# Kernel tuning notes

Measured on AMD Instinct MI355X. Metric: run time of the kernel, lower is better.

## Reference

```python
import jax, jax.numpy as jnp
import numpy as np

D_MODEL = 768
N_HEADS = 12
D_HEAD = D_MODEL // N_HEADS

def setup_inputs() -> dict:
    key = jax.random.key(0)
    ks = jax.random.split(key, 5)
    B, T = 2, 4096
    x = jax.random.normal(ks[0], (B, T, D_MODEL), dtype=jnp.float32)
    s_in = 1.0 / np.sqrt(D_MODEL)
    W_qkv = jax.random.normal(ks[1], (D_MODEL, 3 * D_MODEL), dtype=jnp.float32) * s_in
    b_qkv = jnp.zeros((3 * D_MODEL,), dtype=jnp.float32)
    W_proj = jax.random.normal(ks[2], (D_MODEL, D_MODEL), dtype=jnp.float32) * s_in
    b_proj = jnp.zeros((D_MODEL,), dtype=jnp.float32)
    return {"x": x, "W_qkv": W_qkv, "b_qkv": b_qkv, "W_proj": W_proj, "b_proj": b_proj}

def reference(x, W_qkv, b_qkv, W_proj, b_proj):
    B, T, C = x.shape
    qkv = x @ W_qkv + b_qkv                      # [B,T,3C]
    q, k, v = jnp.split(qkv, 3, axis=-1)
    def heads(t):
        return t.reshape(B, T, N_HEADS, D_HEAD).transpose(0, 2, 1, 3)  # [B,H,T,d]
    q, k, v = heads(q), heads(k), heads(v)
    scale = 1.0 / np.sqrt(D_HEAD)
    att = jnp.einsum('bhqd,bhkd->bhqk', q, k) * scale  # [B,H,T,T]
    causal = jnp.tril(jnp.ones((T, T), dtype=bool))
    att = jnp.where(causal[None, None], att, -jnp.inf)
    att = jax.nn.softmax(att, axis=-1)
    y = jnp.einsum('bhqk,bhkd->bhqd', att, v)          # [B,H,T,d]
    y = y.transpose(0, 2, 1, 3).reshape(B, T, C)
    return y @ W_proj + b_proj
```

## Files before the change

kernel.cpp:

```cpp
#include <hip/hip_runtime.h>
#include <hip/hip_bf16.h>

typedef __bf16 bf16_t;
typedef bf16_t bf16x4 __attribute__((ext_vector_type(4)));
typedef bf16_t bf16x8 __attribute__((ext_vector_type(8)));
typedef float  f32x4  __attribute__((ext_vector_type(4)));

#define TSEQ   4096
#define NBATCH 2
#define DMODEL 768
#define NHEADS 12
#define DHEAD  64
#define NTOK   (NBATCH*TSEQ)
#define NQKV   (3*DMODEL)

#define QSCALE 0.18033688011112042f
#define SMAX 24.0f

__device__ __forceinline__ f32x4 mfma16(bf16x8 a, bf16x8 b, f32x4 c) {
  return __builtin_amdgcn_mfma_f32_16x16x32_bf16(a, b, c, 0, 0, 0);
}

__device__ __forceinline__ void glds16(const bf16_t* g, bf16_t* l) {
  __builtin_amdgcn_global_load_lds(
      (const __attribute__((address_space(1))) void*)g,
      (__attribute__((address_space(3))) void*)l, 16, 0, 0);
}
__device__ __forceinline__ void glds16f(const float* g, float* l) {
  __builtin_amdgcn_global_load_lds(
      (const __attribute__((address_space(1))) void*)g,
      (__attribute__((address_space(3))) void*)l, 16, 0, 0);
}

__global__ __launch_bounds__(256) void k_transpose_cvt2(
    const float* __restrict__ W1, bf16_t* __restrict__ O1,
    const float* __restrict__ W2, bf16_t* __restrict__ O2) {
  __shared__ bf16_t tile[64][66];
  int t = blockIdx.x;
  const float* in; bf16_t* out; int R, C, c0, r0;
  if (t < 432) { in = W1; out = O1; R = DMODEL; C = NQKV;
                 c0 = (t % 36) * 64; r0 = (t / 36) * 64; }
  else { t -= 432; in = W2; out = O2; R = DMODEL; C = DMODEL;
         c0 = (t % 12) * 64; r0 = (t / 12) * 64; }
  const int tid = threadIdx.x;
  const int r = tid >> 2, cb = (tid & 3) * 16;
  const float* ip = in + (long)(r0 + r) * C + c0 + cb;
#pragma unroll
  for (int k = 0; k < 16; k += 4) {
    float4 v = *(const float4*)(ip + k);
    tile[r][cb + k + 0] = (bf16_t)v.x;
    tile[r][cb + k + 1] = (bf16_t)v.y;
    tile[r][cb + k + 2] = (bf16_t)v.z;
    tile[r][cb + k + 3] = (bf16_t)v.w;
  }
  __syncthreads();
  const int c = tid >> 2, rb = (tid & 3) * 16;
  bf16_t* op = out + (long)(c0 + c) * R + r0 + rb;
  bf16x8 v0, v1;
#pragma unroll
  for (int i = 0; i < 8; ++i) { v0[i] = tile[rb + i][c]; v1[i] = tile[rb + 8 + i][c]; }
  *(bf16x8*)(op) = v0;
  *(bf16x8*)(op + 8) = v1;
}

__global__ __launch_bounds__(256) void k_gemm_qkv(
    const float* __restrict__ X, const bf16_t* __restrict__ Bt,
    const float* __restrict__ bias,
    bf16_t* __restrict__ Qo, bf16_t* __restrict__ Ko, bf16_t* __restrict__ Vt) {
  __shared__ __align__(16) float  Asf[2 * 128 * 32];
  __shared__ __align__(16) bf16_t Bs[2 * 128 * 32];
  const int wave = threadIdx.x >> 6;
  const int lane = threadIdx.x & 63;
  const int quad = lane >> 4;
  const int l16  = lane & 15;
  const int m0 = blockIdx.x * 128;
  const int n0 = blockIdx.y * 128;

  const int arow = lane >> 3;
  const int achk = (lane & 7) ^ arow;
  const float* x0 = X + (long)(m0 + wave * 8 + arow) * DMODEL + achk * 4;
  const int srow = lane >> 2;
  const int scol = (lane & 3) * 8;
  const bf16_t* b0 = Bt + (long)(n0 + wave * 16 + srow) * DMODEL + scol;

  f32x4 acc[2][8] = {};

#pragma unroll
  for (int i = 0; i < 4; ++i)
    glds16f(x0 + (long)i * 32 * DMODEL, Asf + (i * 32 + wave * 8) * 32);
  glds16(b0,               Bs + wave * 16 * 32);
  glds16(b0 + 64 * DMODEL, Bs + (64 + wave * 16) * 32);
  __syncthreads();

  const int sk = l16 & 7;
  for (int ks = 0; ks < DMODEL / 32; ++ks) {
    const int p = ks & 1;
    if (ks + 1 < DMODEL / 32) {
      const int k1 = (ks + 1) * 32;
      float*  Asx = (p ? Asf : Asf + 128 * 32);
      bf16_t* Bsx = (p ? Bs : Bs + 128 * 32);
#pragma unroll
      for (int i = 0; i < 4; ++i)
        glds16f(x0 + (long)i * 32 * DMODEL + k1, Asx + (i * 32 + wave * 8) * 32);
      glds16(b0 + k1,               Bsx + wave * 16 * 32);
      glds16(b0 + 64 * DMODEL + k1, Bsx + (64 + wave * 16) * 32);
    }
    const float*  Ap = Asf + p * (128 * 32);
    const bf16_t* Bp = Bs + p * (128 * 32);

    const int r0 = wave * 32 + l16, r1 = r0 + 16;
    f32x4 a0lo = *(const f32x4*)(Ap + r0 * 32 + (((2 * quad)     ^ sk) << 2));
    f32x4 a0hi = *(const f32x4*)(Ap + r0 * 32 + (((2 * quad + 1) ^ sk) << 2));
    f32x4 a1lo = *(const f32x4*)(Ap + r1 * 32 + (((2 * quad)     ^ sk) << 2));
    f32x4 a1hi = *(const f32x4*)(Ap + r1 * 32 + (((2 * quad + 1) ^ sk) << 2));
    bf16x8 af0, af1;
#pragma unroll
    for (int j = 0; j < 4; ++j) {
      af0[j] = (bf16_t)a0lo[j]; af0[4 + j] = (bf16_t)a0hi[j];
      af1[j] = (bf16_t)a1lo[j]; af1[4 + j] = (bf16_t)a1hi[j];
    }
#pragma unroll
    for (int nt = 0; nt < 8; ++nt) {
      bf16x8 bfm = *(const bf16x8*)(Bp + (nt * 16 + l16) * 32 + quad * 8);
      acc[0][nt] = mfma16(af0, bfm, acc[0][nt]);
      acc[1][nt] = mfma16(af1, bfm, acc[1][nt]);
    }
    __syncthreads();
  }

#pragma unroll
  for (int s = 0; s < 2; ++s)
#pragma unroll
    for (int nt = 0; nt < 8; ++nt) {
      const int n = n0 + nt * 16 + l16;
      const float bv = bias[n];
      const int mb = m0 + wave * 32 + s * 16 + quad * 4;
      const int b = mb >> 12;
      const int t = mb & 4095;
      if (n < DMODEL) {
        const int h = n >> 6, d = n & 63;
        bf16_t* qp = Qo + (((long)(b * NHEADS + h) * TSEQ + t) << 6) + d;
#pragma unroll
        for (int j = 0; j < 4; ++j)
          qp[(long)j << 6] = (bf16_t)((acc[s][nt][j] + bv) * QSCALE);
      } else if (n < 2 * DMODEL) {
        const int n2 = n - DMODEL, h = n2 >> 6, d = n2 & 63;
        bf16_t* kp = Ko + (((long)(b * NHEADS + h) * TSEQ + t) << 6) + d;
#pragma unroll
        for (int j = 0; j < 4; ++j)
          kp[(long)j << 6] = (bf16_t)(acc[s][nt][j] + bv);
      } else {
        const int n2 = n - 2 * DMODEL, h = n2 >> 6, d = n2 & 63;
        bf16x4 v;
#pragma unroll
        for (int j = 0; j < 4; ++j) v[j] = (bf16_t)(acc[s][nt][j] + bv);
        *(bf16x4*)(Vt + ((long)(b * NHEADS + h) * DHEAD + d) * TSEQ + t) = v;
      }
    }
}

__global__ __launch_bounds__(256) void k_gemm_proj(
    const bf16_t* __restrict__ P0, const bf16_t* __restrict__ P1,
    const float* __restrict__ L0, const float* __restrict__ L1,
    const bf16_t* __restrict__ Bt, const float* __restrict__ bias,
    float* __restrict__ out) {
  __shared__ __align__(16) bf16_t A0s[2 * 64 * 32];
  __shared__ __align__(16) bf16_t A1s[2 * 64 * 32];
  __shared__ __align__(16) bf16_t Bs[2 * 128 * 32];
  __shared__ float linv[NHEADS * 64];
  const int wave = threadIdx.x >> 6;
  const int lane = threadIdx.x & 63;
  const int quad = lane >> 4;
  const int l16  = lane & 15;
  const int m0 = blockIdx.x * 64;
  const int n0 = blockIdx.y * 128;
  const int b  = m0 >> 12;
  const int t0 = m0 & 4095;

  for (int i = threadIdx.x; i < NHEADS * 64; i += 256) {
    const int h = i >> 6, t = i & 63;
    const long idx = (long)(b * NHEADS + h) * TSEQ + t0 + t;
    linv[i] = 1.f / (L0[idx] + L1[idx]);
  }

  const int srow = lane >> 2;
  const int scol = (lane & 3) * 8;
  const bf16_t* b0 = Bt + (long)(n0 + wave * 16 + srow) * DMODEL + scol;
  const long arowbase = (long)(t0 + wave * 16 + srow);

  f32x4 acc[8] = {};

  {
    const long off = (((long)(b * NHEADS + 0) * TSEQ + arowbase) << 6) + scol;
    glds16(P0 + off, A0s + wave * 16 * 32);
    glds16(P1 + off, A1s + wave * 16 * 32);
  }
  glds16(b0,               Bs + wave * 16 * 32);
  glds16(b0 + 64 * DMODEL, Bs + (64 + wave * 16) * 32);
  __syncthreads();

  for (int ks = 0; ks < DMODEL / 32; ++ks) {
    const int p = ks & 1;
    if (ks + 1 < DMODEL / 32) {
      const int k1 = (ks + 1) * 32;
      const int ksn = ks + 1;
      bf16_t* A0x = (p ? A0s : A0s + 64 * 32);
      bf16_t* A1x = (p ? A1s : A1s + 64 * 32);
      bf16_t* Bsx = (p ? Bs : Bs + 128 * 32);
      const long off = (((long)(b * NHEADS + (ksn >> 1)) * TSEQ + arowbase) << 6)
                       + ((ksn & 1) << 5) + scol;
      glds16(P0 + off, A0x + wave * 16 * 32);
      glds16(P1 + off, A1x + wave * 16 * 32);
      glds16(b0 + k1,               Bsx + wave * 16 * 32);
      glds16(b0 + 64 * DMODEL + k1, Bsx + (64 + wave * 16) * 32);
    }
    const bf16_t* A0p = A0s + p * (64 * 32);
    const bf16_t* A1p = A1s + p * (64 * 32);
    const bf16_t* Bp  = Bs + p * (128 * 32);

    bf16x8 a0 = *(const bf16x8*)(A0p + (wave * 16 + l16) * 32 + quad * 8);
    bf16x8 a1 = *(const bf16x8*)(A1p + (wave * 16 + l16) * 32 + quad * 8);
    const float li = linv[(ks >> 1) * 64 + wave * 16 + l16];
    bf16x8 af;
#pragma unroll
    for (int j = 0; j < 8; ++j)
      af[j] = (bf16_t)(((float)a0[j] + (float)a1[j]) * li);
#pragma unroll
    for (int nt = 0; nt < 8; ++nt) {
      bf16x8 bfm = *(const bf16x8*)(Bp + (nt * 16 + l16) * 32 + quad * 8);
      acc[nt] = mfma16(af, bfm, acc[nt]);
    }
    __syncthreads();
  }

#pragma unroll
  for (int nt = 0; nt < 8; ++nt) {
    const int n = n0 + nt * 16 + l16;
    const float bv = bias[n];
#pragma unroll
    for (int j = 0; j < 4; ++j) {
      const int m = m0 + wave * 16 + quad * 4 + j;
      out[(long)m * DMODEL + n] = acc[nt][j] + bv;
    }
  }
}

__global__ __launch_bounds__(256, 2) void k_attn(
    const bf16_t* __restrict__ Q, const bf16_t* __restrict__ K,
    const bf16_t* __restrict__ Vt,
    bf16_t* __restrict__ P0, bf16_t* __restrict__ P1,
    float* __restrict__ L0, float* __restrict__ L1) {
  __shared__ __align__(16) bf16_t kbuf[2][64 * 64];
  __shared__ __align__(16) bf16_t vbuf[2][64 * 64];
  const int wave = threadIdx.x >> 6;
  const int lane = threadIdx.x & 63;
  const int quad = lane >> 4;
  const int l16  = lane & 15;
  const int bh = blockIdx.x;
  const int qt = 15 - (blockIdx.y >> 1);
  const int sp = blockIdx.y & 1;
  const int half = 2 * qt + 2;
  const int c0 = sp ? half : 0;
  const int niter = half;
  bf16_t* Pp = sp ? P1 : P0;
  float*  Lp = sp ? L1 : L0;

  const bf16_t* Qh = Q + ((long)bh * TSEQ << 6);
  const bf16_t* Kh = K + ((long)bh * TSEQ << 6);
  const bf16_t* Vh = Vt + (long)bh * DHEAD * TSEQ;

  const int qbase = qt * 256 + wave * 64;

  bf16x8 qf[4][2];
#pragma unroll
  for (int s = 0; s < 4; ++s) {
    const bf16_t* qrow = Qh + ((long)(qbase + s * 16 + l16) << 6);
    qf[s][0] = *(const bf16x8*)(qrow + quad * 8);
    qf[s][1] = *(const bf16x8*)(qrow + 32 + quad * 8);
  }

  f32x4 acc[4][4] = {};
  float lS[4] = {0.f, 0.f, 0.f, 0.f};
  const f32x4 minit = {-SMAX, -SMAX, -SMAX, -SMAX};

  const int kperm = ((l16 >> 2) << 3) + (l16 & 3);
  const int swl = l16 & 7;
  const int srow = lane >> 3;
  const int cV = (lane & 7) ^ (srow & 7);
  const int cK0 = (lane & 7) ^ (srow & 3);
  const int cK1 = cK0 ^ 4;
  const int r0a = wave * 16, r0b = wave * 16 + 8;

  {
    const int k00 = c0 << 6;
    glds16(Kh + ((long)(k00 + r0a + srow) << 6) + cK0 * 8, &kbuf[0][r0a * 64]);
    glds16(Kh + ((long)(k00 + r0b + srow) << 6) + cK1 * 8, &kbuf[0][r0b * 64]);
    glds16(Vh + (long)(r0a + srow) * TSEQ + k00 + cV * 8,  &vbuf[0][r0a * 64]);
    glds16(Vh + (long)(r0b + srow) * TSEQ + k00 + cV * 8,  &vbuf[0][r0b * 64]);
  }
  __syncthreads();

  for (int ci = 0; ci < niter; ++ci) {
    const int p = ci & 1;
    const int k0 = (c0 + ci) << 6;
    if (ci + 1 < niter) {
      const int k1 = k0 + 64;
      glds16(Kh + ((long)(k1 + r0a + srow) << 6) + cK0 * 8, &kbuf[1 - p][r0a * 64]);
      glds16(Kh + ((long)(k1 + r0b + srow) << 6) + cK1 * 8, &kbuf[1 - p][r0b * 64]);
      glds16(Vh + (long)(r0a + srow) * TSEQ + k1 + cV * 8,  &vbuf[1 - p][r0a * 64]);
      glds16(Vh + (long)(r0b + srow) * TSEQ + k1 + cV * 8,  &vbuf[1 - p][r0b * 64]);
    }
    const bf16_t* kb = kbuf[p];
    const bf16_t* vb = vbuf[p];

#pragma unroll
    for (int g = 0; g < 2; ++g) {
      const int rw0 = (g * 32 + kperm) * 64;
      const int rw1 = (g * 32 + 4 + kperm) * 64;
      bf16x8 kf00 = *(const bf16x8*)(kb + rw0 + ((quad ^ swl) << 3));
      bf16x8 kf01 = *(const bf16x8*)(kb + rw0 + (((quad + 4) ^ swl) << 3));
      bf16x8 kf10 = *(const bf16x8*)(kb + rw1 + ((quad ^ swl) << 3));
      bf16x8 kf11 = *(const bf16x8*)(kb + rw1 + (((quad + 4) ^ swl) << 3));
      const bool domask = (k0 + g * 32 + 31 > qbase);

      bf16x8 pf[4];
#pragma unroll
      for (int s = 0; s < 4; ++s) {
        f32x4 st0 = minit, st1 = minit;
        st0 = mfma16(kf00, qf[s][0], st0);
        st0 = mfma16(kf01, qf[s][1], st0);
        st1 = mfma16(kf10, qf[s][0], st1);
        st1 = mfma16(kf11, qf[s][1], st1);
        if (domask) {
          const int qS = qbase + s * 16 + l16;
          const int kb0 = k0 + g * 32 + quad * 8;
#pragma unroll
          for (int j = 0; j < 4; ++j) {
            if (kb0 + j > qS)     st0[j] = -1e30f;
            if (kb0 + 4 + j > qS) st1[j] = -1e30f;
          }
        }
        float rs = 0.f;
#pragma unroll
        for (int j = 0; j < 4; ++j) {
          float e0 = __builtin_amdgcn_exp2f(st0[j]);
          float e1 = __builtin_amdgcn_exp2f(st1[j]);
          rs += e0 + e1;
          pf[s][j]     = (bf16_t)e0;
          pf[s][4 + j] = (bf16_t)e1;
        }
        lS[s] += rs;
      }
#pragma unroll
      for (int dt = 0; dt < 4; ++dt) {
        const int row = dt * 16 + l16;
        bf16x8 vf = *(const bf16x8*)(vb + row * 64 + ((((g << 2) + quad) ^ swl) << 3));
#pragma unroll
        for (int s = 0; s < 4; ++s)
          acc[s][dt] = mfma16(vf, pf[s], acc[s][dt]);
      }
    }
    __syncthreads();
  }

#pragma unroll
  for (int s = 0; s < 4; ++s) {
    lS[s] += __shfl_xor(lS[s], 16);
    lS[s] += __shfl_xor(lS[s], 32);
  }
#pragma unroll
  for (int s = 0; s < 4; ++s) {
    const int qS = qbase + s * 16 + l16;
    bf16_t* prow = Pp + (((long)bh * TSEQ + qS) << 6);
#pragma unroll
    for (int dt = 0; dt < 4; ++dt) {
      bf16x4 w;
#pragma unroll
      for (int j = 0; j < 4; ++j) w[j] = (bf16_t)acc[s][dt][j];
      *(bf16x4*)(prow + dt * 16 + quad * 4) = w;
    }
    if (quad == 0) Lp[(long)bh * TSEQ + qS] = lS[s];
  }
}

extern "C" void kernel_launch(void* const* d_in, const int* in_sizes, int n_in,
                              void* d_out, int out_size, void* d_ws, size_t ws_size,
                              hipStream_t stream) {
  (void)in_sizes; (void)n_in; (void)out_size; (void)ws_size;
  const float* x     = (const float*)d_in[0];
  const float* Wqkv  = (const float*)d_in[1];
  const float* bqkv  = (const float*)d_in[2];
  const float* Wproj = (const float*)d_in[3];
  const float* bproj = (const float*)d_in[4];
  float* out = (float*)d_out;

  char* ws = (char*)d_ws;
  bf16_t* wqkv_t  = (bf16_t*)ws; ws += (long)NQKV * DMODEL * 2;
  bf16_t* wproj_t = (bf16_t*)ws; ws += (long)DMODEL * DMODEL * 2;
  bf16_t* Qb      = (bf16_t*)ws; ws += (long)NTOK * DMODEL * 2;
  bf16_t* Kb      = (bf16_t*)ws; ws += (long)NTOK * DMODEL * 2;
  bf16_t* Vtb     = (bf16_t*)ws; ws += (long)NTOK * DMODEL * 2;
  bf16_t* P0b     = (bf16_t*)ws; ws += (long)NTOK * DMODEL * 2;
  bf16_t* P1b     = (bf16_t*)ws; ws += (long)NTOK * DMODEL * 2;
  float*  L0b     = (float*)ws;  ws += (long)NHEADS * NBATCH * TSEQ * 4;
  float*  L1b     = (float*)ws;  ws += (long)NHEADS * NBATCH * TSEQ * 4;

  k_transpose_cvt2<<<576, 256, 0, stream>>>(Wqkv, wqkv_t, Wproj, wproj_t);
  k_gemm_qkv<<<dim3(NTOK / 128, NQKV / 128), 256, 0, stream>>>(x, wqkv_t, bqkv, Qb, Kb, Vtb);
  k_attn<<<dim3(NBATCH * NHEADS, 32), 256, 0, stream>>>(Qb, Kb, Vtb, P0b, P1b, L0b, L1b);
  k_gemm_proj<<<dim3(NTOK / 64, DMODEL / 128), 256, 0, stream>>>(
      P0b, P1b, L0b, L1b, wproj_t, bproj, out);
}
```

Measured before the change: 226.6 us.

## Pre-convert X to bf16 in prep kernel and share bf16 GEMM core

X is now converted from fp32 to bf16 in a separate pass inside the weight-prep kernel, so the QKV GEMM loads bf16 A tiles instead of fp32 tiles and converting them per iteration. This halves A-tile LDS footprint and per-step load traffic, and removes the in-loop conversions. The grid is also swapped so consecutive blocks walk N first, which may improve reuse of A rows in cache. The cost is an extra read of X and a write plus re-read of the bf16 copy.

```diff
diff --git a/kernel.cpp b/kernel.cpp
--- a/kernel.cpp
+++ b/kernel.cpp
@@ -26,23 +26,29 @@
       (const __attribute__((address_space(1))) void*)g,
       (__attribute__((address_space(3))) void*)l, 16, 0, 0);
 }
-__device__ __forceinline__ void glds16f(const float* g, float* l) {
-  __builtin_amdgcn_global_load_lds(
-      (const __attribute__((address_space(1))) void*)g,
-      (__attribute__((address_space(3))) void*)l, 16, 0, 0);
-}
-
-__global__ __launch_bounds__(256) void k_transpose_cvt2(
+
+__global__ __launch_bounds__(256) void k_prep(
     const float* __restrict__ W1, bf16_t* __restrict__ O1,
-    const float* __restrict__ W2, bf16_t* __restrict__ O2) {
+    const float* __restrict__ W2, bf16_t* __restrict__ O2,
+    const float* __restrict__ X, bf16_t* __restrict__ Xb) {
+  int t = blockIdx.x;
+  const int tid = threadIdx.x;
+  if (t >= 576) {
+    const long base = (long)(t - 576) * 2048 + tid * 8;
+    float4 v0 = *(const float4*)(X + base);
+    float4 v1 = *(const float4*)(X + base + 4);
+    bf16x8 r;
+    r[0] = (bf16_t)v0.x; r[1] = (bf16_t)v0.y; r[2] = (bf16_t)v0.z; r[3] = (bf16_t)v0.w;
+    r[4] = (bf16_t)v1.x; r[5] = (bf16_t)v1.y; r[6] = (bf16_t)v1.z; r[7] = (bf16_t)v1.w;
+    *(bf16x8*)(Xb + base) = r;
+    return;
+  }
   __shared__ bf16_t tile[64][66];
-  int t = blockIdx.x;
   const float* in; bf16_t* out; int R, C, c0, r0;
   if (t < 432) { in = W1; out = O1; R = DMODEL; C = NQKV;
                  c0 = (t % 36) * 64; r0 = (t / 36) * 64; }
   else { t -= 432; in = W2; out = O2; R = DMODEL; C = DMODEL;
          c0 = (t % 12) * 64; r0 = (t / 12) * 64; }
-  const int tid = threadIdx.x;
   const int r = tid >> 2, cb = (tid & 3) * 16;
   const float* ip = in + (long)(r0 + r) * C + c0 + cb;
 #pragma unroll
@@ -63,70 +69,67 @@
   *(bf16x8*)(op + 8) = v1;
 }
 
+__device__ __forceinline__ void gemm_core(
+    const bf16_t* __restrict__ A, const bf16_t* __restrict__ Bt,
+    int m0, int n0, bf16_t* As, bf16_t* Bs, f32x4 acc[2][8]) {
+  const int tid  = threadIdx.x;
+  const int wave = tid >> 6;
+  const int lane = tid & 63;
+  const int quad = lane >> 4;
+  const int l16  = lane & 15;
+  const int srow = lane >> 2;
+  const int scol = (lane & 3) * 8;
+
+  const bf16_t* a0 = A + (long)(m0 + wave * 16 + srow) * DMODEL + scol;
+  const bf16_t* b0 = Bt + (long)(n0 + wave * 16 + srow) * DMODEL + scol;
+
+  glds16(a0,               As + wave * 16 * 32);
+  glds16(a0 + 64 * DMODEL, As + (64 + wave * 16) * 32);
+  glds16(b0,               Bs + wave * 16 * 32);
+  glds16(b0 + 64 * DMODEL, Bs + (64 + wave * 16) * 32);
+  __syncthreads();
+
+  for (int ks = 0; ks < DMODEL / 32; ++ks) {
+    const int p = ks & 1;
+    if (ks + 1 < DMODEL / 32) {
+      const int k1 = (ks + 1) * 32;
+      bf16_t* Asx = (p ? As : As + 128 * 32);
+      bf16_t* Bsx = (p ? Bs : Bs + 128 * 32);
+      glds16(a0 + k1,               Asx + wave * 16 * 32);
+      glds16(a0 + 64 * DMODEL + k1, Asx + (64 + wave * 16) * 32);
+      glds16(b0 + k1,               Bsx + wave * 16 * 32);
+      glds16(b0 + 64 * DMODEL + k1, Bsx + (64 + wave * 16) * 32);
+    }
+    const bf16_t* Ap = As + p * (128 * 32);
+    const bf16_t* Bp = Bs + p * (128 * 32);
+
+    bf16x8 af0 = *(const bf16x8*)(Ap + (wave * 32 + l16) * 32 + quad * 8);
+    bf16x8 af1 = *(const bf16x8*)(Ap + (wave * 32 + 16 + l16) * 32 + quad * 8);
+#pragma unroll
+    for (int nt = 0; nt < 8; ++nt) {
+      bf16x8 bfm = *(const bf16x8*)(Bp + (nt * 16 + l16) * 32 + quad * 8);
+      acc[0][nt] = mfma16(af0, bfm, acc[0][nt]);
+      acc[1][nt] = mfma16(af1, bfm, acc[1][nt]);
+    }
+    __syncthreads();
+  }
+}
+
 __global__ __launch_bounds__(256) void k_gemm_qkv(
-    const float* __restrict__ X, const bf16_t* __restrict__ Bt,
+    const bf16_t* __restrict__ A, const bf16_t* __restrict__ Bt,
     const float* __restrict__ bias,
     bf16_t* __restrict__ Qo, bf16_t* __restrict__ Ko, bf16_t* __restrict__ Vt) {
-  __shared__ __align__(16) float  Asf[2 * 128 * 32];
+  __shared__ __align__(16) bf16_t As[2 * 128 * 32];
   __shared__ __align__(16) bf16_t Bs[2 * 128 * 32];
   const int wave = threadIdx.x >> 6;
   const int lane = threadIdx.x & 63;
   const int quad = lane >> 4;
   const int l16  = lane & 15;
-  const int m0 = blockIdx.x * 128;
-  const int n0 = blockIdx.y * 128;
-
-  const int arow = lane >> 3;
-  const int achk = (lane & 7) ^ arow;
-  const float* x0 = X + (long)(m0 + wave * 8 + arow) * DMODEL + achk * 4;
-  const int srow = lane >> 2;
-  const int scol = (lane & 3) * 8;
-  const bf16_t* b0 = Bt + (long)(n0 + wave * 16 + srow) * DMODEL + scol;
+  const int m0 = blockIdx.y * 128;
+  const int n0 = blockIdx.x * 128;
 
   f32x4 acc[2][8] = {};
-
-#pragma unroll
-  for (int i = 0; i < 4; ++i)
-    glds16f(x0 + (long)i * 32 * DMODEL, Asf + (i * 32 + wave * 8) * 32);
-  glds16(b0,               Bs + wave * 16 * 32);
-  glds16(b0 + 64 * DMODEL, Bs + (64 + wave * 16) * 32);
-  __syncthreads();
-
-  const int sk = l16 & 7;
-  for (int ks = 0; ks < DMODEL / 32; ++ks) {
-    const int p = ks & 1;
-    if (ks + 1 < DMODEL / 32) {
-      const int k1 = (ks + 1) * 32;
-      float*  Asx = (p ? Asf : Asf + 128 * 32);
-      bf16_t* Bsx = (p ? Bs : Bs + 128 * 32);
-#pragma unroll
-      for (int i = 0; i < 4; ++i)
-        glds16f(x0 + (long)i * 32 * DMODEL + k1, Asx + (i * 32 + wave * 8) * 32);
-      glds16(b0 + k1,               Bsx + wave * 16 * 32);
-      glds16(b0 + 64 * DMODEL + k1, Bsx + (64 + wave * 16) * 32);
-    }
-    const float*  Ap = Asf + p * (128 * 32);
-    const bf16_t* Bp = Bs + p * (128 * 32);
-
-    const int r0 = wave * 32 + l16, r1 = r0 + 16;
-    f32x4 a0lo = *(const f32x4*)(Ap + r0 * 32 + (((2 * quad)     ^ sk) << 2));
-    f32x4 a0hi = *(const f32x4*)(Ap + r0 * 32 + (((2 * quad + 1) ^ sk) << 2));
-    f32x4 a1lo = *(const f32x4*)(Ap + r1 * 32 + (((2 * quad)     ^ sk) << 2));
-    f32x4 a1hi = *(const f32x4*)(Ap + r1 * 32 + (((2 * quad + 1) ^ sk) << 2));
-    bf16x8 af0, af1;
-#pragma unroll
-    for (int j = 0; j < 4; ++j) {
-      af0[j] = (bf16_t)a0lo[j]; af0[4 + j] = (bf16_t)a0hi[j];
-      af1[j] = (bf16_t)a1lo[j]; af1[4 + j] = (bf16_t)a1hi[j];
-    }
-#pragma unroll
-    for (int nt = 0; nt < 8; ++nt) {
-      bf16x8 bfm = *(const bf16x8*)(Bp + (nt * 16 + l16) * 32 + quad * 8);
-      acc[0][nt] = mfma16(af0, bfm, acc[0][nt]);
-      acc[1][nt] = mfma16(af1, bfm, acc[1][nt]);
-    }
-    __syncthreads();
-  }
+  gemm_core(A, Bt, m0, n0, As, Bs, acc);
 
 #pragma unroll
   for (int s = 0; s < 2; ++s)
@@ -395,6 +398,7 @@
   float* out = (float*)d_out;
 
   char* ws = (char*)d_ws;
+  bf16_t* Xb      = (bf16_t*)ws; ws += (long)NTOK * DMODEL * 2;
   bf16_t* wqkv_t  = (bf16_t*)ws; ws += (long)NQKV * DMODEL * 2;
   bf16_t* wproj_t = (bf16_t*)ws; ws += (long)DMODEL * DMODEL * 2;
   bf16_t* Qb      = (bf16_t*)ws; ws += (long)NTOK * DMODEL * 2;
@@ -405,8 +409,8 @@
   float*  L0b     = (float*)ws;  ws += (long)NHEADS * NBATCH * TSEQ * 4;
   float*  L1b     = (float*)ws;  ws += (long)NHEADS * NBATCH * TSEQ * 4;
 
-  k_transpose_cvt2<<<576, 256, 0, stream>>>(Wqkv, wqkv_t, Wproj, wproj_t);
-  k_gemm_qkv<<<dim3(NTOK / 128, NQKV / 128), 256, 0, stream>>>(x, wqkv_t, bqkv, Qb, Kb, Vtb);
+  k_prep<<<3648, 256, 0, stream>>>(Wqkv, wqkv_t, Wproj, wproj_t, x, Xb);
+  k_gemm_qkv<<<dim3(NQKV / 128, NTOK / 128), 256, 0, stream>>>(Xb, wqkv_t, bqkv, Qb, Kb, Vtb);
   k_attn<<<dim3(NBATCH * NHEADS, 32), 256, 0, stream>>>(Qb, Kb, Vtb, P0b, P1b, L0b, L1b);
   k_gemm_proj<<<dim3(NTOK / 64, DMODEL / 128), 256, 0, stream>>>(
       P0b, P1b, L0b, L1b, wproj_t, bproj, out);
```

Result: slower. 233.2 us (+2.9%).
